# Kernel tuning notes

Hardware: AMD Instinct MI355X
Metric: run time of the kernel (lower is better)

Reference implementation:

```python
import jax, jax.numpy as jnp
import numpy as np

WIN = 7          # window width (matches init win_size)
EPS = 1e-4       # Tikhonov regularization for the per-pixel normal equations
NF = 8           # features: [1, depth, albedo(3), normal(3)]


def _box_sum(x, win):
    # (windows are clipped at image borders, as in the CUDA kernel).
    ndim = x.ndim
    wdims = (1,) * (ndim - 2) + (win, win)
    return jax.lax.reduce_window(x, 0.0, jax.lax.add, wdims, (1,) * ndim, 'SAME')


def setup_inputs() -> dict:
    key = jax.random.key(0)
    k1, k2, k3, k4 = jax.random.split(key, 4)
    B, H, W = 1, 1024, 1024
    inp = jax.random.normal(k1, (B, 3, H, W), dtype=jnp.float32)
    depth = jax.random.uniform(k2, (B, 1, H, W), dtype=jnp.float32)
    albedo = jax.random.uniform(k3, (B, 3, H, W), dtype=jnp.float32)
    normal = jax.random.normal(k4, (B, 3, H, W), dtype=jnp.float32)
    normal = normal / (jnp.linalg.norm(normal, axis=1, keepdims=True) + 1e-6)
    return {"input": inp, "depth": depth, "albedo": albedo, "normal": normal}


def reference(input, depth, albedo, normal):
    B, C, H, W = input.shape
    ones = jnp.ones((B, 1, H, W), dtype=input.dtype)
    # Feature maps f: [B, 8, H, W] = [1, depth, albedo, normal]
    f = jnp.concatenate([ones, depth, albedo, normal], axis=1)

    # Per-pixel normal equations via box-filtered feature products.
    # AtA[b,i,j,h,w] = sum_{window} f_i * f_j   -> [B, 8, 8, H, W]
    AtA = _box_sum(f[:, :, None] * f[:, None], WIN)
    # AtY[b,i,c,h,w] = sum_{window} f_i * y_c   -> [B, 8, 3, H, W]
    AtY = _box_sum(f[:, :, None] * input[:, None], WIN)

    AtA = jnp.moveaxis(AtA, (1, 2), (3, 4))  # [B, H, W, 8, 8]
    AtY = jnp.moveaxis(AtY, (1, 2), (3, 4))  # [B, H, W, 8, 3]
    AtA = AtA + EPS * jnp.eye(NF, dtype=input.dtype)

    # Batched 8x8 solves, one per pixel.
    beta = jnp.linalg.solve(AtA, AtY)  # [B, H, W, 8, 3]

    # Evaluate fitted model at the center pixel's features.
    out = jnp.einsum('bhwfc,bfhw->bchw', beta, f)
    return out
```

## Files before the change

### kernel.cpp

```cpp
#include <hip/hip_runtime.h>
#include <math.h>

#define HH 1024
#define WW 1024
#define OUTW 58
#define RPB 4
#define WPB 4
#define OFF(i) ((i)*8 - (i)*((i)-1)/2)


template<int CTRL>
__device__ __forceinline__ float dpp0(float x) {
    return __int_as_float(
        __builtin_amdgcn_update_dpp(0, __float_as_int(x), CTRL, 0xf, 0xf, true));
}
__device__ __forceinline__ float wshr1(float x) { return dpp0<0x138>(x); }

__device__ __forceinline__ float frsqrt_fast(float s) {
    float r = __builtin_amdgcn_rsqf(s);
    r = r * (1.5f - 0.5f * s * r * r);
    return r;
}

__global__ __launch_bounds__(WPB * 64, 2) void ls_sep_kernel(
    const float* __restrict__ inp,
    const float* __restrict__ dep,
    const float* __restrict__ alb,
    const float* __restrict__ nrm,
    float* __restrict__ out)
{
    const int L  = threadIdx.x & 63;
    const int wv = threadIdx.x >> 6;
    const int HW = HH * WW;
    const int x  = OUTW * blockIdx.x - 3 + L;
    const int y0 = (RPB * WPB) * blockIdx.y + RPB * wv;
    const int px = x - 3;

    const int xc    = min(max(x, 0), WW - 1);
    const float xok = (x >= 0 && x < WW) ? 1.f : 0.f;

    float C[60];
    #pragma unroll
    for (int k = 0; k < 60; k++) C[k] = 0.f;

    auto acc_row = [&](int yy, float sgn) {
        const int yc = min(max(yy, 0), HH - 1);
        const float ok = (yy >= 0 && yy < HH) ? xok : 0.f;
        const int p = yc * WW + xc;
        float fv[8], yv[3];
        fv[0] = 1.f;
        fv[1] = dep[p];
        fv[2] = alb[p];
        fv[3] = alb[p + HW];
        fv[4] = alb[p + 2 * HW];
        fv[5] = nrm[p];
        fv[6] = nrm[p + HW];
        fv[7] = nrm[p + 2 * HW];
        yv[0] = inp[p];
        yv[1] = inp[p + HW];
        yv[2] = inp[p + 2 * HW];
        const float s = sgn * ok;
        float fs[8];
        #pragma unroll
        for (int i = 0; i < 8; i++) fs[i] = fv[i] * s;
        int k = 0;
        #pragma unroll
        for (int i = 0; i < 8; i++)
            #pragma unroll
            for (int j = i; j < 8; j++) { C[k] = fmaf(fs[i], fv[j], C[k]); k++; }
        #pragma unroll
        for (int i = 0; i < 8; i++)
            #pragma unroll
            for (int c = 0; c < 3; c++)
                C[36 + i * 3 + c] = fmaf(fs[i], yv[c], C[36 + i * 3 + c]);
    };

    #pragma unroll 1
    for (int yy = y0 - 4; yy < y0 + 3; yy++) acc_row(yy, 1.f);

    const int idxm4 = ((L - 4) & 63) << 2;
    const int pxc = min(max(px, 0), WW - 1);
    const bool do_store = (L >= 6) && (px < WW);

    #pragma unroll 1
    for (int y = y0; y < y0 + RPB; y++) {
        acc_row(y + 3, 1.f);
        acc_row(y - 4, -1.f);

        float S[60];
        #pragma unroll
        for (int k = 0; k < 60; k++) {
            const float xv = C[k];
            const float w1 = wshr1(xv);
            const float t1 = xv + w1;
            const float w2 = wshr1(w1);
            const float t3 = t1 + w2;
            const float w3 = wshr1(w2);
            const float t2 = t3 + w3;
            const float pm = __int_as_float(
                __builtin_amdgcn_ds_bpermute(idxm4, __float_as_int(t3)));
            S[k] = t2 + pm;
        }

        const int pc = y * WW + pxc;
        float cf[8];
        cf[0] = 1.f;
        cf[1] = dep[pc];
        cf[2] = alb[pc];
        cf[3] = alb[pc + HW];
        cf[4] = alb[pc + 2 * HW];
        cf[5] = nrm[pc];
        cf[6] = nrm[pc + HW];
        cf[7] = nrm[pc + 2 * HW];

        float A[36];
        #pragma unroll
        for (int k = 0; k < 36; k++) A[k] = S[k];
        #pragma unroll
        for (int i = 0; i < 8; i++) A[OFF(i)] += 1.0e-4f;

        float invd[8];
        #pragma unroll
        for (int i = 0; i < 8; i++) {
            float s = A[OFF(i)];
            #pragma unroll
            for (int k2 = 0; k2 < i; k2++) {
                const float u = A[OFF(k2) + i - k2];
                s = fmaf(-u, u, s);
            }
            const float id = frsqrt_fast(s);
            invd[i] = id;
            #pragma unroll
            for (int j = i + 1; j < 8; j++) {
                float s2 = A[OFF(i) + j - i];
                #pragma unroll
                for (int k2 = 0; k2 < i; k2++)
                    s2 = fmaf(-A[OFF(k2) + i - k2], A[OFF(k2) + j - k2], s2);
                A[OFF(i) + j - i] = s2 * id;
            }
        }

        float z[8];
        #pragma unroll
        for (int i = 0; i < 8; i++) {
            float s = cf[i];
            #pragma unroll
            for (int k2 = 0; k2 < i; k2++)
                s = fmaf(-A[OFF(k2) + i - k2], z[k2], s);
            z[i] = s * invd[i];
        }
        float w[8];
        #pragma unroll
        for (int i = 7; i >= 0; i--) {
            float s = z[i];
            #pragma unroll
            for (int j = i + 1; j < 8; j++)
                s = fmaf(-A[OFF(i) + j - i], w[j], s);
            w[i] = s * invd[i];
        }

        if (do_store) {
            const int p = y * WW + px;
            #pragma unroll
            for (int c = 0; c < 3; c++) {
                float r = 0.f;
                #pragma unroll
                for (int i = 0; i < 8; i++)
                    r = fmaf(w[i], S[36 + i * 3 + c], r);
                out[c * HW + p] = r;
            }
        }
    }
}

extern "C" void kernel_launch(void* const* d_in, const int* in_sizes, int n_in,
                              void* d_out, int out_size, void* d_ws, size_t ws_size,
                              hipStream_t stream) {
    const float* inp = (const float*)d_in[0];
    const float* dep = (const float*)d_in[1];
    const float* alb = (const float*)d_in[2];
    const float* nrm = (const float*)d_in[3];
    float* out = (float*)d_out;
    dim3 grid((WW + OUTW - 1) / OUTW, HH / (RPB * WPB));
    ls_sep_kernel<<<grid, dim3(WPB * 64), 0, stream>>>(inp, dep, alb, nrm, out);
}
```

Measured before the change: 128.8 us.

## Prefetch next window rows during solve and switch Cholesky to LDL^T with reciprocals

The sliding-window row loads for the next output row are issued before the per-pixel factorization, and their accumulation is deferred to the end of the iteration, so global memory latency overlaps the solve arithmetic. The initial window is shifted to match this update order. The Cholesky factorization with rsqrt is replaced by an LDL^T-style elimination that uses a fast reciprocal, which removes the square roots and reshapes the dependency chains. Holding the prefetched rows live across the solve raises register pressure, and the numerical behavior of the solve changes slightly.

Measured after the change: 143.4 us. 11.3% more time.

```diff
diff --git a/kernel.cpp b/kernel.cpp
--- a/kernel.cpp
+++ b/kernel.cpp
@@ -16,10 +16,9 @@
 }
 __device__ __forceinline__ float wshr1(float x) { return dpp0<0x138>(x); }
 
-__device__ __forceinline__ float frsqrt_fast(float s) {
-    float r = __builtin_amdgcn_rsqf(s);
-    r = r * (1.5f - 0.5f * s * r * r);
-    return r;
+__device__ __forceinline__ float frcp_fast(float s) {
+    float r = __builtin_amdgcn_rcpf(s);
+    return r * fmaf(-s, r, 2.0f);
 }
 
 __global__ __launch_bounds__(WPB * 64, 2) void ls_sep_kernel(
@@ -43,31 +42,29 @@
     #pragma unroll
     for (int k = 0; k < 60; k++) C[k] = 0.f;
 
-    auto acc_row = [&](int yy, float sgn) {
+    auto load_row = [&](int yy, float fv[7], float yv[3]) -> float {
         const int yc = min(max(yy, 0), HH - 1);
         const float ok = (yy >= 0 && yy < HH) ? xok : 0.f;
         const int p = yc * WW + xc;
-        float fv[8], yv[3];
-        fv[0] = 1.f;
-        fv[1] = dep[p];
-        fv[2] = alb[p];
-        fv[3] = alb[p + HW];
-        fv[4] = alb[p + 2 * HW];
-        fv[5] = nrm[p];
-        fv[6] = nrm[p + HW];
-        fv[7] = nrm[p + 2 * HW];
-        yv[0] = inp[p];
-        yv[1] = inp[p + HW];
-        yv[2] = inp[p + 2 * HW];
-        const float s = sgn * ok;
+        fv[0] = dep[p];
+        fv[1] = alb[p]; fv[2] = alb[p + HW]; fv[3] = alb[p + 2 * HW];
+        fv[4] = nrm[p]; fv[5] = nrm[p + HW]; fv[6] = nrm[p + 2 * HW];
+        yv[0] = inp[p]; yv[1] = inp[p + HW]; yv[2] = inp[p + 2 * HW];
+        return ok;
+    };
+    auto acc_regs = [&](const float fv[7], const float yv[3], float s) {
+        float f8[8];
+        f8[0] = 1.f;
+        #pragma unroll
+        for (int i = 0; i < 7; i++) f8[i + 1] = fv[i];
         float fs[8];
         #pragma unroll
-        for (int i = 0; i < 8; i++) fs[i] = fv[i] * s;
+        for (int i = 0; i < 8; i++) fs[i] = f8[i] * s;
         int k = 0;
         #pragma unroll
         for (int i = 0; i < 8; i++)
             #pragma unroll
-            for (int j = i; j < 8; j++) { C[k] = fmaf(fs[i], fv[j], C[k]); k++; }
+            for (int j = i; j < 8; j++) { C[k] = fmaf(fs[i], f8[j], C[k]); k++; }
         #pragma unroll
         for (int i = 0; i < 8; i++)
             #pragma unroll
@@ -76,7 +73,11 @@
     };
 
     #pragma unroll 1
-    for (int yy = y0 - 4; yy < y0 + 3; yy++) acc_row(yy, 1.f);
+    for (int yy = y0 - 3; yy <= y0 + 3; yy++) {
+        float fv[7], yv[3];
+        const float ok = load_row(yy, fv, yv);
+        acc_regs(fv, yv, ok);
+    }
 
     const int idxm4 = ((L - 4) & 63) << 2;
     const int pxc = min(max(px, 0), WW - 1);
@@ -84,9 +85,6 @@
 
     #pragma unroll 1
     for (int y = y0; y < y0 + RPB; y++) {
-        acc_row(y + 3, 1.f);
-        acc_row(y - 4, -1.f);
-
         float S[60];
         #pragma unroll
         for (int k = 0; k < 60; k++) {
@@ -102,61 +100,53 @@
             S[k] = t2 + pm;
         }
 
+        float fE[7], yE[3], fL[7], yL[3];
+        const float okE = load_row(y + 4, fE, yE);
+        const float okL = load_row(y - 3, fL, yL);
+
         const int pc = y * WW + pxc;
         float cf[8];
         cf[0] = 1.f;
         cf[1] = dep[pc];
-        cf[2] = alb[pc];
-        cf[3] = alb[pc + HW];
-        cf[4] = alb[pc + 2 * HW];
-        cf[5] = nrm[pc];
-        cf[6] = nrm[pc + HW];
-        cf[7] = nrm[pc + 2 * HW];
+        cf[2] = alb[pc]; cf[3] = alb[pc + HW]; cf[4] = alb[pc + 2 * HW];
+        cf[5] = nrm[pc]; cf[6] = nrm[pc + HW]; cf[7] = nrm[pc + 2 * HW];
 
-        float A[36];
+        float W[36];
         #pragma unroll
-        for (int k = 0; k < 36; k++) A[k] = S[k];
+        for (int k = 0; k < 36; k++) W[k] = S[k];
         #pragma unroll
-        for (int i = 0; i < 8; i++) A[OFF(i)] += 1.0e-4f;
+        for (int i = 0; i < 8; i++) W[OFF(i)] += 1.0e-4f;
 
-        float invd[8];
+        float idv[8];
         #pragma unroll
         for (int i = 0; i < 8; i++) {
-            float s = A[OFF(i)];
             #pragma unroll
-            for (int k2 = 0; k2 < i; k2++) {
-                const float u = A[OFF(k2) + i - k2];
-                s = fmaf(-u, u, s);
+            for (int k = 0; k < i; k++) {
+                const float c = W[OFF(k) + i - k] * idv[k];
+                #pragma unroll
+                for (int j = i; j < 8; j++)
+                    W[OFF(i) + j - i] = fmaf(-c, W[OFF(k) + j - k], W[OFF(i) + j - i]);
             }
-            const float id = frsqrt_fast(s);
-            invd[i] = id;
-            #pragma unroll
-            for (int j = i + 1; j < 8; j++) {
-                float s2 = A[OFF(i) + j - i];
-                #pragma unroll
-                for (int k2 = 0; k2 < i; k2++)
-                    s2 = fmaf(-A[OFF(k2) + i - k2], A[OFF(k2) + j - k2], s2);
-                A[OFF(i) + j - i] = s2 * id;
-            }
+            idv[i] = frcp_fast(W[OFF(i)]);
         }
 
-        float z[8];
+        float vt[8];
         #pragma unroll
         for (int i = 0; i < 8; i++) {
             float s = cf[i];
             #pragma unroll
-            for (int k2 = 0; k2 < i; k2++)
-                s = fmaf(-A[OFF(k2) + i - k2], z[k2], s);
-            z[i] = s * invd[i];
+            for (int k = 0; k < i; k++)
+                s = fmaf(-W[OFF(k) + i - k], vt[k], s);
+            vt[i] = s * idv[i];
         }
         float w[8];
         #pragma unroll
         for (int i = 7; i >= 0; i--) {
-            float s = z[i];
+            float t = 0.f;
             #pragma unroll
             for (int j = i + 1; j < 8; j++)
-                s = fmaf(-A[OFF(i) + j - i], w[j], s);
-            w[i] = s * invd[i];
+                t = fmaf(W[OFF(i) + j - i], w[j], t);
+            w[i] = fmaf(-idv[i], t, vt[i]);
         }
 
         if (do_store) {
@@ -170,6 +160,9 @@
                 out[c * HW + p] = r;
             }
         }
+
+        acc_regs(fE, yE, okE);
+        acc_regs(fL, yL, -okL);
     }
 }
 
```
